# Kernel tuning notes

Measured on AMD Instinct MI355X. Metric: run time of the kernel, lower is better.

Reference implementation:

```python
import jax, jax.numpy as jnp
import numpy as np

N_NODES = 50000
N_EDGES = 600000
IN_DIM = 128
HID_DIM = 128
OUT_DIM = 128
N_GRAPHS = 64


def _glorot(key, shape):
    lim = np.sqrt(6.0 / (shape[0] + shape[1]))
    return jax.random.uniform(key, shape, jnp.float32, -lim, lim)


def setup_inputs() -> dict:
    key = jax.random.key(0)
    ks = jax.random.split(key, 8)
    h = jax.random.normal(ks[0], (N_NODES, IN_DIM), jnp.float32)
    src = jax.random.randint(ks[1], (N_EDGES,), 0, N_NODES, jnp.int64)
    dst = jax.random.randint(ks[2], (N_EDGES,), 0, N_NODES, jnp.int64)
    graph_ids = jnp.sort(jax.random.randint(ks[3], (N_NODES,), 0, N_GRAPHS, jnp.int64))
    W1 = _glorot(ks[4], (IN_DIM, HID_DIM)); b1 = jnp.zeros((HID_DIM,), jnp.float32)
    W2 = _glorot(ks[5], (HID_DIM, HID_DIM)); b2 = jnp.zeros((HID_DIM,), jnp.float32)
    W3 = _glorot(ks[6], (HID_DIM, OUT_DIM)); b3 = jnp.zeros((OUT_DIM,), jnp.float32)
    return {"h": h, "src": src, "dst": dst, "graph_ids": graph_ids,
            "W1": W1, "b1": b1, "W2": W2, "b2": b2, "W3": W3, "b3": b3,
            "n_graphs": N_GRAPHS}


def _graph_conv(h, src, dst, norm_src, norm_dst, W, b):
    # DGL GraphConv, norm='both': D_dst^{-1/2} A^T D_src^{-1/2} h W + b
    m = h * norm_src[:, None]                                   # [N, d]
    agg = jax.ops.segment_sum(m[src], dst, num_segments=h.shape[0])  # [N, d]
    return (agg * norm_dst[:, None]) @ W + b


def reference(h, src, dst, graph_ids, W1, b1, W2, b2, W3, b3, n_graphs):
    n = h.shape[0]
    ones = jnp.ones((src.shape[0],), h.dtype)
    out_deg = jnp.clip(jax.ops.segment_sum(ones, src, num_segments=n), 1.0)
    in_deg = jnp.clip(jax.ops.segment_sum(ones, dst, num_segments=n), 1.0)
    norm_src = out_deg ** -0.5
    norm_dst = in_deg ** -0.5

    x = jax.nn.relu(_graph_conv(h, src, dst, norm_src, norm_dst, W1, b1))
    x = jax.nn.relu(_graph_conv(x, src, dst, norm_src, norm_dst, W2, b2))
    x = jax.nn.relu(_graph_conv(x, src, dst, norm_src, norm_dst, W3, b3))

    # dgl.mean_nodes: per-graph mean over nodes
    gsum = jax.ops.segment_sum(x, graph_ids, num_segments=n_graphs)          # [G, d]
    gcnt = jax.ops.segment_sum(jnp.ones((n,), x.dtype), graph_ids, num_segments=n_graphs)
    return gsum / jnp.clip(gcnt, 1.0)[:, None]
```

## Files before the change

### kernel.cpp

```cpp
#include <hip/hip_runtime.h>
#include <hip/hip_fp16.h>


#define DIM 128
#define GRAPHS 64

typedef _Float16 half8 __attribute__((ext_vector_type(8)));
typedef _Float16 half4 __attribute__((ext_vector_type(4)));
typedef float floatx4 __attribute__((ext_vector_type(4)));

#define HIST_R 4
#define HIST_S 64
#define NPR 12500
#define LDSW (NPR / 2)

__global__ __launch_bounds__(256) void k_hist(const int* __restrict__ src,
                                              const int* __restrict__ dst,
                                              unsigned* __restrict__ partial, int E) {
    __shared__ unsigned hist[LDSW];
    int b = blockIdx.x;
    int a = b / (HIST_R * HIST_S);
    int r = (b / HIST_S) % HIST_R;
    int s = b % HIST_S;
    const int* arr = a ? dst : src;
    for (int i = threadIdx.x; i < LDSW; i += 256) hist[i] = 0;
    __syncthreads();
    int chunk = (E + HIST_S - 1) / HIST_S;
    int e0 = s * chunk;
    int e1 = min(e0 + chunk, E);
    unsigned base = (unsigned)(r * NPR);
    for (int i = e0 + threadIdx.x; i < e1; i += 256) {
        unsigned n = (unsigned)arr[i] - base;
        if (n < NPR) atomicAdd(&hist[n >> 1], 1u << ((n & 1) * 16));
    }
    __syncthreads();
    unsigned* outp = partial + ((size_t)(a * HIST_R + r) * HIST_S + s) * LDSW;
    for (int i = threadIdx.x; i < LDSW; i += 256) outp[i] = hist[i];
}

__global__ __launch_bounds__(256) void k_hist_merge(const unsigned* __restrict__ partial,
                                                    float* __restrict__ ns,
                                                    float* __restrict__ nd,
                                                    int* __restrict__ inc,
                                                    int* __restrict__ bsum, int N) {
    __shared__ int sred[256];
    int nb = (N + 255) / 256;
    int isDst = (blockIdx.x < nb) ? 1 : 0;
    int cb = isDst ? blockIdx.x : blockIdx.x - nb;
    int n = cb * 256 + threadIdx.x;
    int deg = 0;
    if (n < N) {
        int a = isDst ? 1 : 0;
        int r = n / NPR;
        int w = (n % NPR) >> 1;
        int field = (n & 1) * 16;
        const unsigned* p = partial + ((size_t)(a * HIST_R + r) * HIST_S) * LDSW + w;
        unsigned sum = 0;
#pragma unroll
        for (int s = 0; s < HIST_S; ++s) sum += p[(size_t)s * LDSW];
        deg = (int)((sum >> field) & 0xFFFFu);
        float nrm = rsqrtf(fmaxf((float)deg, 1.0f));
        if (isDst) { nd[n] = nrm; inc[n] = deg; }
        else       { ns[n] = nrm; }
    }
    if (isDst) {
        sred[threadIdx.x] = deg;
        __syncthreads();
        for (int off = 128; off > 0; off >>= 1) {
            if (threadIdx.x < off) sred[threadIdx.x] += sred[threadIdx.x + off];
            __syncthreads();
        }
        if (threadIdx.x == 0) bsum[cb] = sred[0];
    }
}

__global__ __launch_bounds__(256) void k_scan_write(const int* __restrict__ inc,
                                                    const int* __restrict__ bsum,
                                                    const unsigned* __restrict__ partial,
                                                    int* __restrict__ row_ptr,
                                                    int* __restrict__ cur,
                                                    float* __restrict__ gsum, int N) {
    __shared__ int sb[256];
    __shared__ int s[256];
    __shared__ int exs[256];
    int nb = (N + 255) / 256;
    int t = threadIdx.x;

    int bv = (t < nb) ? bsum[t] : 0;
    sb[t] = bv;
    __syncthreads();
    for (int off = 1; off < 256; off <<= 1) {
        int u = (t >= off) ? sb[t - off] : 0;
        __syncthreads();
        sb[t] += u;
        __syncthreads();
    }
    int excl = sb[t] - bv;
    __syncthreads();
    sb[t] = excl;
    __syncthreads();
    int blockBase = sb[blockIdx.x];

    int B = blockIdx.x * 256;
    int i = B + t;
    int v = (i < N) ? inc[i] : 0;
    s[t] = v;
    __syncthreads();
    for (int off = 1; off < 256; off <<= 1) {
        int u = (t >= off) ? s[t - off] : 0;
        __syncthreads();
        s[t] += u;
        __syncthreads();
    }
    int ex = blockBase + s[t] - v;
    exs[t] = ex;
    if (i < N) row_ptr[i] = ex;
    if (i == N - 1) row_ptr[N] = ex + v;
    if (blockIdx.x == 0) {
        for (int j = t; j < GRAPHS * DIM; j += 256) gsum[j] = 0.0f;
    }
    __syncthreads();

    if (t < 128) {
        int n0 = B + 2 * t;
        if (n0 < N) {
            int r = n0 / NPR;
            int w = (n0 % NPR) >> 1;
            const unsigned* p = partial + ((size_t)(HIST_R + r) * HIST_S) * LDSW + w;
            int run0 = exs[2 * t];
            int run1 = exs[2 * t + 1];
            int* c = cur + (size_t)r * HIST_S * NPR + 2 * w;
#pragma unroll
            for (int sl = 0; sl < HIST_S; ++sl) {
                c[(size_t)sl * NPR + 0] = run0;
                c[(size_t)sl * NPR + 1] = run1;
                unsigned hv = p[(size_t)sl * LDSW];
                run0 += (int)(hv & 0xFFFFu);
                run1 += (int)(hv >> 16);
            }
        }
    }
}

__global__ __launch_bounds__(256) void k_fill2(const int* __restrict__ src,
                                               const int* __restrict__ dst,
                                               const int* __restrict__ cur,
                                               int* __restrict__ csr, int E) {
    __shared__ int lcur[NPR];
    int r = blockIdx.x / HIST_S;
    int s = blockIdx.x % HIST_S;
    const int* cs = cur + (size_t)(r * HIST_S + s) * NPR;
    for (int i = threadIdx.x; i < NPR; i += 256) lcur[i] = cs[i];
    __syncthreads();
    int chunk = (E + HIST_S - 1) / HIST_S;
    int e0 = s * chunk;
    int e1 = min(e0 + chunk, E);
    unsigned base = (unsigned)(r * NPR);
    for (int i = e0 + threadIdx.x; i < e1; i += 256) {
        unsigned d = (unsigned)dst[i] - base;
        if (d < NPR) {
            int p = atomicAdd(&lcur[d], 1);
            csr[p] = src[i];
        }
    }
}

__global__ void k_prep(const float4* __restrict__ h, const float* __restrict__ ns,
                       uint2* __restrict__ A,
                       const float* __restrict__ W1, const float* __restrict__ W2,
                       const float* __restrict__ W3, _Float16* __restrict__ Wt1,
                       _Float16* __restrict__ Wt2, _Float16* __restrict__ Wt3, int N) {
    int i = blockIdx.x * blockDim.x + threadIdx.x;
    int nf4 = N * 32;
    if (i < nf4) {
        int n = i >> 5;
        float s = ns[n];
        float4 v = h[i];
        __half2 p0 = __floats2half2_rn(v.x * s, v.y * s);
        __half2 p1 = __floats2half2_rn(v.z * s, v.w * s);
        uint2 o;
        o.x = *(unsigned*)&p0;
        o.y = *(unsigned*)&p1;
        A[i] = o;
    } else {
        int j = i - nf4;
        if (j < 3 * 16384) {
            int which = j >> 14;
            int local = j & 16383;
            int k = local >> 7;
            int n = local & 127;
            const float* W = (which == 0) ? W1 : (which == 1) ? W2 : W3;
            _Float16* Wt = (which == 0) ? Wt1 : (which == 1) ? Wt2 : Wt3;
            Wt[(size_t)n * DIM + k] = (_Float16)W[local];
        }
    }
}

__global__ __launch_bounds__(256) void k_agg(const uint2* __restrict__ A,
                                             const int* __restrict__ row_ptr,
                                             const int* __restrict__ csr,
                                             const float* __restrict__ nd,
                                             uint2* __restrict__ Bh, int N) {
    int gtid = blockIdx.x * blockDim.x + threadIdx.x;
    int node = gtid >> 6;
    int lane = threadIdx.x & 63;
    if (node >= N) return;
    int e0 = row_ptr[node];
    int e1 = row_ptr[node + 1];
    int half = lane >> 5;
    int l8 = lane & 31;
    float ax = 0.f, ay = 0.f, az = 0.f, aw = 0.f;

    for (int base = e0; base < e1; base += 16) {
        int vl = csr[min(base + (lane & 15), e1 - 1)];
        int idx[8];
        uint2 u[8];
#pragma unroll
        for (int j = 0; j < 8; ++j) {
            idx[j] = __shfl(vl, 2 * j + half);
        }
#pragma unroll
        for (int j = 0; j < 8; ++j) {
            u[j] = A[(size_t)idx[j] * 32 + l8];
        }
#pragma unroll
        for (int j = 0; j < 8; ++j) {
            int ee = base + 2 * j + half;
            if (ee < e1) {
                __half2 p0 = *(__half2*)&u[j].x;
                __half2 p1 = *(__half2*)&u[j].y;
                float2 f0 = __half22float2(p0);
                float2 f1 = __half22float2(p1);
                ax += f0.x; ay += f0.y; az += f1.x; aw += f1.y;
            }
        }
    }

    ax += __shfl_xor(ax, 32);
    ay += __shfl_xor(ay, 32);
    az += __shfl_xor(az, 32);
    aw += __shfl_xor(aw, 32);

    if (half == 0) {
        float scale = nd[node];
        __half2 p0 = __floats2half2_rn(ax * scale, ay * scale);
        __half2 p1 = __floats2half2_rn(az * scale, aw * scale);
        uint2 o;
        o.x = *(unsigned*)&p0;
        o.y = *(unsigned*)&p1;
        Bh[(size_t)node * 32 + l8] = o;
    }
}

template <bool SCALE_NS>
__global__ __launch_bounds__(256) void k_gemm_t(
    const _Float16* __restrict__ Bin, const _Float16* __restrict__ Wt,
    const float* __restrict__ bias, const float* __restrict__ ns,
    _Float16* __restrict__ Xout, int N) {
    int tid = threadIdx.x;
    int wave = tid >> 6;
    int lane = tid & 63;
    int quad = lane >> 4;
    int l16 = lane & 15;
    int node = blockIdx.x * 64 + wave * 16 + l16;

    half8 b[4];
#pragma unroll
    for (int q = 0; q < 4; ++q) {
        if (node < N) {
            b[q] = *(const half8*)&Bin[(size_t)node * DIM + q * 32 + quad * 8];
        } else {
            b[q] = half8{0, 0, 0, 0, 0, 0, 0, 0};
        }
    }

    floatx4 acc[8];
#pragma unroll
    for (int c = 0; c < 8; ++c) acc[c] = floatx4{0.f, 0.f, 0.f, 0.f};

#pragma unroll
    for (int c = 0; c < 8; ++c) {
#pragma unroll
        for (int q = 0; q < 4; ++q) {
            half8 a = *(const half8*)&Wt[(size_t)(c * 16 + l16) * DIM + q * 32 + quad * 8];
            acc[c] = __builtin_amdgcn_mfma_f32_16x16x32_f16(a, b[q], acc[c], 0, 0, 0);
        }
    }

    if (node < N) {
        float s = SCALE_NS ? ns[node] : 1.0f;
#pragma unroll
        for (int c = 0; c < 8; ++c) {
            float4 b4 = *(const float4*)&bias[c * 16 + quad * 4];
            half4 o;
            o[0] = (_Float16)(fmaxf(acc[c][0] + b4.x, 0.0f) * s);
            o[1] = (_Float16)(fmaxf(acc[c][1] + b4.y, 0.0f) * s);
            o[2] = (_Float16)(fmaxf(acc[c][2] + b4.z, 0.0f) * s);
            o[3] = (_Float16)(fmaxf(acc[c][3] + b4.w, 0.0f) * s);
            *(half4*)&Xout[(size_t)node * DIM + c * 16 + quad * 4] = o;
        }
    }
}

#define PBINS 8
__global__ __launch_bounds__(256) void k_gemm_pool(
    const _Float16* __restrict__ Bin, const _Float16* __restrict__ Wt,
    const float* __restrict__ bias, const int* __restrict__ gid,
    float* __restrict__ gsum, int N) {
    __shared__ float lsum[PBINS * DIM];
    int tid = threadIdx.x;
    for (int i = tid; i < PBINS * DIM; i += 256) lsum[i] = 0.0f;
    int wave = tid >> 6;
    int lane = tid & 63;
    int quad = lane >> 4;
    int l16 = lane & 15;
    int r0 = blockIdx.x * 64;
    int node = r0 + wave * 16 + l16;
    int nodec = min(node, N - 1);

    half8 b[4];
#pragma unroll
    for (int q = 0; q < 4; ++q) {
        if (node < N) {
            b[q] = *(const half8*)&Bin[(size_t)node * DIM + q * 32 + quad * 8];
        } else {
            b[q] = half8{0, 0, 0, 0, 0, 0, 0, 0};
        }
    }

    floatx4 acc[8];
#pragma unroll
    for (int c = 0; c < 8; ++c) acc[c] = floatx4{0.f, 0.f, 0.f, 0.f};
    __syncthreads();

#pragma unroll
    for (int c = 0; c < 8; ++c) {
#pragma unroll
        for (int q = 0; q < 4; ++q) {
            half8 a = *(const half8*)&Wt[(size_t)(c * 16 + l16) * DIM + q * 32 + quad * 8];
            acc[c] = __builtin_amdgcn_mfma_f32_16x16x32_f16(a, b[q], acc[c], 0, 0, 0);
        }
    }

    int g = gid[nodec];
    int g0b = gid[r0];
    int gEb = gid[min(r0 + 63, N - 1)];
    bool ldsPath = (gEb - g0b) < PBINS;
    int gF = __shfl(g, 0);
    int gL = __shfl(g, 15);
    bool uni = (gF == gL);
    float valid = (node < N) ? 1.0f : 0.0f;

#pragma unroll
    for (int c = 0; c < 8; ++c) {
        float4 b4 = *(const float4*)&bias[c * 16 + quad * 4];
        float bv[4] = {b4.x, b4.y, b4.z, b4.w};
#pragma unroll
        for (int r = 0; r < 4; ++r) {
            float v = fmaxf(acc[c][r] + bv[r], 0.0f) * valid;
            int f = c * 16 + quad * 4 + r;
            if (ldsPath) {
                if (uni) {
                    v += __shfl_xor(v, 1);
                    v += __shfl_xor(v, 2);
                    v += __shfl_xor(v, 4);
                    v += __shfl_xor(v, 8);
                    if (l16 == 0) atomicAdd(&lsum[(gF - g0b) * DIM + f], v);
                } else {
                    if (node < N) atomicAdd(&lsum[(g - g0b) * DIM + f], v);
                }
            } else {
                if (node < N) atomicAdd(&gsum[(size_t)g * DIM + f], v);
            }
        }
    }
    __syncthreads();
    if (ldsPath) {
        int ng = gEb - g0b + 1;
        for (int i = tid; i < ng * DIM; i += 256) {
            float sv = lsum[i];
            if (sv != 0.0f) atomicAdd(&gsum[(size_t)g0b * DIM + i], sv);
        }
    }
}

__global__ void k_finalize(const float* __restrict__ gsum, const int* __restrict__ gid,
                           float* __restrict__ out, int N, int G) {
    int i = blockIdx.x * blockDim.x + threadIdx.x;
    if (i < G * DIM) {
        int g = i >> 7;
        int lo = 0, hi = N;
        while (lo < hi) { int m = (lo + hi) >> 1; if (gid[m] < g) lo = m + 1; else hi = m; }
        int lo2 = lo, hi2 = N;
        while (lo2 < hi2) { int m = (lo2 + hi2) >> 1; if (gid[m] < g + 1) lo2 = m + 1; else hi2 = m; }
        float c = fmaxf((float)(lo2 - lo), 1.0f);
        out[i] = gsum[i] / c;
    }
}

extern "C" void kernel_launch(void* const* d_in, const int* in_sizes, int n_in,
                              void* d_out, int out_size, void* d_ws, size_t ws_size,
                              hipStream_t stream) {
    const float* h   = (const float*)d_in[0];
    const int*   src = (const int*)d_in[1];
    const int*   dst = (const int*)d_in[2];
    const int*   gid = (const int*)d_in[3];
    const float* W1  = (const float*)d_in[4];
    const float* b1  = (const float*)d_in[5];
    const float* W2  = (const float*)d_in[6];
    const float* b2  = (const float*)d_in[7];
    const float* W3  = (const float*)d_in[8];
    const float* b3  = (const float*)d_in[9];

    const int N = in_sizes[0] / DIM;
    const int E = in_sizes[1];
    const int G = GRAPHS;
    float* out = (float*)d_out;

    char* ws = (char*)d_ws;
    size_t off = 0;
    auto alloc = [&](size_t bytes) -> void* {
        void* p = ws + off;
        off += (bytes + 255) & ~(size_t)255;
        return p;
    };
    const int nb = (N + 255) / 256;
    uint2* Ah0     = (uint2*)alloc((size_t)N * DIM * 2);
    uint2* Ah1     = (uint2*)alloc((size_t)N * DIM * 2);
    uint2* Bh      = (uint2*)alloc((size_t)N * DIM * 2);
    _Float16* Wt1  = (_Float16*)alloc((size_t)DIM * DIM * 2);
    _Float16* Wt2  = (_Float16*)alloc((size_t)DIM * DIM * 2);
    _Float16* Wt3  = (_Float16*)alloc((size_t)DIM * DIM * 2);
    float* ns      = (float*)alloc((size_t)N * 4);
    float* nd      = (float*)alloc((size_t)N * 4);
    int*   inc     = (int*)alloc((size_t)N * 4);
    unsigned* partial = (unsigned*)alloc((size_t)2 * HIST_R * HIST_S * LDSW * 4);
    int*   cur     = (int*)alloc((size_t)HIST_R * HIST_S * NPR * 4);
    int*   row_ptr = (int*)alloc((size_t)(N + 1) * 4);
    int*   csr     = (int*)alloc((size_t)E * 4);
    float* gsum    = (float*)alloc((size_t)G * DIM * 4);
    int*   bsum    = (int*)alloc((size_t)nb * 4);

    k_hist<<<2 * HIST_R * HIST_S, 256, 0, stream>>>(src, dst, partial, E);
    k_hist_merge<<<2 * nb, 256, 0, stream>>>(partial, ns, nd, inc, bsum, N);
    k_scan_write<<<nb, 256, 0, stream>>>(inc, bsum, partial, row_ptr, cur, gsum, N);
    k_fill2<<<HIST_R * HIST_S, 256, 0, stream>>>(src, dst, cur, csr, E);

    int prepThreads = N * 32 + 3 * 16384;
    k_prep<<<(prepThreads + 255) / 256, 256, 0, stream>>>((const float4*)h, ns, Ah0,
                                                          W1, W2, W3, Wt1, Wt2, Wt3, N);

    int aggBlocks  = (N * 64 + 255) / 256;
    int gemmBlocks = (N + 63) / 64;

    k_agg<<<aggBlocks, 256, 0, stream>>>(Ah0, row_ptr, csr, nd, Bh, N);
    k_gemm_t<true><<<gemmBlocks, 256, 0, stream>>>((const _Float16*)Bh, Wt1, b1, ns, (_Float16*)Ah1, N);
    k_agg<<<aggBlocks, 256, 0, stream>>>(Ah1, row_ptr, csr, nd, Bh, N);
    k_gemm_t<true><<<gemmBlocks, 256, 0, stream>>>((const _Float16*)Bh, Wt2, b2, ns, (_Float16*)Ah0, N);
    k_agg<<<aggBlocks, 256, 0, stream>>>(Ah0, row_ptr, csr, nd, Bh, N);
    k_gemm_pool<<<gemmBlocks, 256, 0, stream>>>((const _Float16*)Bh, Wt3, b3, gid, gsum, N);

    k_finalize<<<(G * DIM + 255) / 256, 256, 0, stream>>>(gsum, gid, out, N, G);
}
```

Before: 310.2 us.

## Fuse neighbor aggregation and MFMA GEMM into one per-layer kernel via LDS tile

Each layer's gather-aggregate and dense transform are merged into a single kernel. Each block aggregates 16 nodes (4 per wave) into an LDS tile, then wave 0 runs the MFMA GEMM from that tile and writes the activated output or pools it. This drops the intermediate Bh buffer round-trip through global memory and halves the layer kernel launches. The cost is less parallelism: each wave now walks 4 nodes serially, and 3 of 4 waves sit idle during the GEMM. The pooling path also loses its LDS pre-reduction, so it issues more global atomics.

```diff
diff --git a/kernel.cpp b/kernel.cpp
--- a/kernel.cpp
+++ b/kernel.cpp
@@ -196,79 +196,84 @@
     }
 }
 
-__global__ __launch_bounds__(256) void k_agg(const uint2* __restrict__ A,
-                                             const int* __restrict__ row_ptr,
-                                             const int* __restrict__ csr,
-                                             const float* __restrict__ nd,
-                                             uint2* __restrict__ Bh, int N) {
-    int gtid = blockIdx.x * blockDim.x + threadIdx.x;
-    int node = gtid >> 6;
-    int lane = threadIdx.x & 63;
-    if (node >= N) return;
-    int e0 = row_ptr[node];
-    int e1 = row_ptr[node + 1];
-    int half = lane >> 5;
-    int l8 = lane & 31;
-    float ax = 0.f, ay = 0.f, az = 0.f, aw = 0.f;
-
-    for (int base = e0; base < e1; base += 16) {
-        int vl = csr[min(base + (lane & 15), e1 - 1)];
-        int idx[8];
-        uint2 u[8];
-#pragma unroll
-        for (int j = 0; j < 8; ++j) {
-            idx[j] = __shfl(vl, 2 * j + half);
-        }
-#pragma unroll
-        for (int j = 0; j < 8; ++j) {
-            u[j] = A[(size_t)idx[j] * 32 + l8];
-        }
-#pragma unroll
-        for (int j = 0; j < 8; ++j) {
-            int ee = base + 2 * j + half;
-            if (ee < e1) {
-                __half2 p0 = *(__half2*)&u[j].x;
-                __half2 p1 = *(__half2*)&u[j].y;
-                float2 f0 = __half22float2(p0);
-                float2 f1 = __half22float2(p1);
-                ax += f0.x; ay += f0.y; az += f1.x; aw += f1.y;
-            }
-        }
-    }
-
-    ax += __shfl_xor(ax, 32);
-    ay += __shfl_xor(ay, 32);
-    az += __shfl_xor(az, 32);
-    aw += __shfl_xor(aw, 32);
-
-    if (half == 0) {
-        float scale = nd[node];
-        __half2 p0 = __floats2half2_rn(ax * scale, ay * scale);
-        __half2 p1 = __floats2half2_rn(az * scale, aw * scale);
-        uint2 o;
-        o.x = *(unsigned*)&p0;
-        o.y = *(unsigned*)&p1;
-        Bh[(size_t)node * 32 + l8] = o;
-    }
-}
-
-template <bool SCALE_NS>
-__global__ __launch_bounds__(256) void k_gemm_t(
-    const _Float16* __restrict__ Bin, const _Float16* __restrict__ Wt,
-    const float* __restrict__ bias, const float* __restrict__ ns,
-    _Float16* __restrict__ Xout, int N) {
+#define TSTRIDE 136
+
+template <bool SCALE_NS, bool POOL>
+__global__ __launch_bounds__(256) void k_layer(
+    const uint2* __restrict__ A, const int* __restrict__ row_ptr,
+    const int* __restrict__ csr, const float* __restrict__ nd,
+    const _Float16* __restrict__ Wt, const float* __restrict__ bias,
+    const float* __restrict__ ns, const int* __restrict__ gid,
+    _Float16* __restrict__ Xout, float* __restrict__ gsum, int N) {
+    __shared__ _Float16 tile[16 * TSTRIDE];
     int tid = threadIdx.x;
     int wave = tid >> 6;
     int lane = tid & 63;
+    int r0 = blockIdx.x * 16;
+
+    int half = lane >> 5;
+    int l8 = lane & 31;
+#pragma unroll 1
+    for (int i = 0; i < 4; ++i) {
+        int nl = wave * 4 + i;
+        int node = r0 + nl;
+        if (node >= N) break;
+        int e0 = row_ptr[node];
+        int e1 = row_ptr[node + 1];
+        float ax = 0.f, ay = 0.f, az = 0.f, aw = 0.f;
+
+        for (int base = e0; base < e1; base += 16) {
+            int vl = csr[min(base + (lane & 15), e1 - 1)];
+            int idx[8];
+            uint2 u[8];
+#pragma unroll
+            for (int j = 0; j < 8; ++j) {
+                idx[j] = __shfl(vl, 2 * j + half);
+            }
+#pragma unroll
+            for (int j = 0; j < 8; ++j) {
+                u[j] = A[(size_t)idx[j] * 32 + l8];
+            }
+#pragma unroll
+            for (int j = 0; j < 8; ++j) {
+                int ee = base + 2 * j + half;
+                if (ee < e1) {
+                    __half2 p0 = *(__half2*)&u[j].x;
+                    __half2 p1 = *(__half2*)&u[j].y;
+                    float2 f0 = __half22float2(p0);
+                    float2 f1 = __half22float2(p1);
+                    ax += f0.x; ay += f0.y; az += f1.x; aw += f1.y;
+                }
+            }
+        }
+
+        ax += __shfl_xor(ax, 32);
+        ay += __shfl_xor(ay, 32);
+        az += __shfl_xor(az, 32);
+        aw += __shfl_xor(aw, 32);
+
+        if (half == 0) {
+            float scale = nd[node];
+            __half2 p0 = __floats2half2_rn(ax * scale, ay * scale);
+            __half2 p1 = __floats2half2_rn(az * scale, aw * scale);
+            uint2 o;
+            o.x = *(unsigned*)&p0;
+            o.y = *(unsigned*)&p1;
+            *(uint2*)&tile[nl * TSTRIDE + l8 * 4] = o;
+        }
+    }
+    __syncthreads();
+
+    if (wave != 0) return;
     int quad = lane >> 4;
     int l16 = lane & 15;
-    int node = blockIdx.x * 64 + wave * 16 + l16;
+    int node = r0 + l16;
 
     half8 b[4];
 #pragma unroll
     for (int q = 0; q < 4; ++q) {
         if (node < N) {
-            b[q] = *(const half8*)&Bin[(size_t)node * DIM + q * 32 + quad * 8];
+            b[q] = *(const half8*)&tile[l16 * TSTRIDE + q * 32 + quad * 8];
         } else {
             b[q] = half8{0, 0, 0, 0, 0, 0, 0, 0};
         }
@@ -287,99 +292,46 @@
         }
     }
 
-    if (node < N) {
-        float s = SCALE_NS ? ns[node] : 1.0f;
+    if (!POOL) {
+        if (node < N) {
+            float s = SCALE_NS ? ns[node] : 1.0f;
+#pragma unroll
+            for (int c = 0; c < 8; ++c) {
+                float4 b4 = *(const float4*)&bias[c * 16 + quad * 4];
+                half4 o;
+                o[0] = (_Float16)(fmaxf(acc[c][0] + b4.x, 0.0f) * s);
+                o[1] = (_Float16)(fmaxf(acc[c][1] + b4.y, 0.0f) * s);
+                o[2] = (_Float16)(fmaxf(acc[c][2] + b4.z, 0.0f) * s);
+                o[3] = (_Float16)(fmaxf(acc[c][3] + b4.w, 0.0f) * s);
+                *(half4*)&Xout[(size_t)node * DIM + c * 16 + quad * 4] = o;
+            }
+        }
+    } else {
+        int nodec = min(node, N - 1);
+        int g = gid[nodec];
+        int gF = __shfl(g, 0);
+        int gL = __shfl(g, 15);
+        bool uni = (gF == gL);
+        float valid = (node < N) ? 1.0f : 0.0f;
+
 #pragma unroll
         for (int c = 0; c < 8; ++c) {
             float4 b4 = *(const float4*)&bias[c * 16 + quad * 4];
-            half4 o;
-            o[0] = (_Float16)(fmaxf(acc[c][0] + b4.x, 0.0f) * s);
-            o[1] = (_Float16)(fmaxf(acc[c][1] + b4.y, 0.0f) * s);
-            o[2] = (_Float16)(fmaxf(acc[c][2] + b4.z, 0.0f) * s);
-            o[3] = (_Float16)(fmaxf(acc[c][3] + b4.w, 0.0f) * s);
-            *(half4*)&Xout[(size_t)node * DIM + c * 16 + quad * 4] = o;
-        }
-    }
-}
-
-#define PBINS 8
-__global__ __launch_bounds__(256) void k_gemm_pool(
-    const _Float16* __restrict__ Bin, const _Float16* __restrict__ Wt,
-    const float* __restrict__ bias, const int* __restrict__ gid,
-    float* __restrict__ gsum, int N) {
-    __shared__ float lsum[PBINS * DIM];
-    int tid = threadIdx.x;
-    for (int i = tid; i < PBINS * DIM; i += 256) lsum[i] = 0.0f;
-    int wave = tid >> 6;
-    int lane = tid & 63;
-    int quad = lane >> 4;
-    int l16 = lane & 15;
-    int r0 = blockIdx.x * 64;
-    int node = r0 + wave * 16 + l16;
-    int nodec = min(node, N - 1);
-
-    half8 b[4];
-#pragma unroll
-    for (int q = 0; q < 4; ++q) {
-        if (node < N) {
-            b[q] = *(const half8*)&Bin[(size_t)node * DIM + q * 32 + quad * 8];
-        } else {
-            b[q] = half8{0, 0, 0, 0, 0, 0, 0, 0};
-        }
-    }
-
-    floatx4 acc[8];
-#pragma unroll
-    for (int c = 0; c < 8; ++c) acc[c] = floatx4{0.f, 0.f, 0.f, 0.f};
-    __syncthreads();
-
-#pragma unroll
-    for (int c = 0; c < 8; ++c) {
-#pragma unroll
-        for (int q = 0; q < 4; ++q) {
-            half8 a = *(const half8*)&Wt[(size_t)(c * 16 + l16) * DIM + q * 32 + quad * 8];
-            acc[c] = __builtin_amdgcn_mfma_f32_16x16x32_f16(a, b[q], acc[c], 0, 0, 0);
-        }
-    }
-
-    int g = gid[nodec];
-    int g0b = gid[r0];
-    int gEb = gid[min(r0 + 63, N - 1)];
-    bool ldsPath = (gEb - g0b) < PBINS;
-    int gF = __shfl(g, 0);
-    int gL = __shfl(g, 15);
-    bool uni = (gF == gL);
-    float valid = (node < N) ? 1.0f : 0.0f;
-
-#pragma unroll
-    for (int c = 0; c < 8; ++c) {
-        float4 b4 = *(const float4*)&bias[c * 16 + quad * 4];
-        float bv[4] = {b4.x, b4.y, b4.z, b4.w};
-#pragma unroll
-        for (int r = 0; r < 4; ++r) {
-            float v = fmaxf(acc[c][r] + bv[r], 0.0f) * valid;
-            int f = c * 16 + quad * 4 + r;
-            if (ldsPath) {
+            float bv[4] = {b4.x, b4.y, b4.z, b4.w};
+#pragma unroll
+            for (int r = 0; r < 4; ++r) {
+                float v = fmaxf(acc[c][r] + bv[r], 0.0f) * valid;
+                int f = c * 16 + quad * 4 + r;
                 if (uni) {
                     v += __shfl_xor(v, 1);
                     v += __shfl_xor(v, 2);
                     v += __shfl_xor(v, 4);
                     v += __shfl_xor(v, 8);
-                    if (l16 == 0) atomicAdd(&lsum[(gF - g0b) * DIM + f], v);
+                    if (l16 == 0) atomicAdd(&gsum[(size_t)gF * DIM + f], v);
                 } else {
-                    if (node < N) atomicAdd(&lsum[(g - g0b) * DIM + f], v);
+                    if (node < N) atomicAdd(&gsum[(size_t)g * DIM + f], v);
                 }
-            } else {
-                if (node < N) atomicAdd(&gsum[(size_t)g * DIM + f], v);
-            }
-        }
-    }
-    __syncthreads();
-    if (ldsPath) {
-        int ng = gEb - g0b + 1;
-        for (int i = tid; i < ng * DIM; i += 256) {
-            float sv = lsum[i];
-            if (sv != 0.0f) atomicAdd(&gsum[(size_t)g0b * DIM + i], sv);
+            }
         }
     }
 }
@@ -427,7 +379,6 @@
     const int nb = (N + 255) / 256;
     uint2* Ah0     = (uint2*)alloc((size_t)N * DIM * 2);
     uint2* Ah1     = (uint2*)alloc((size_t)N * DIM * 2);
-    uint2* Bh      = (uint2*)alloc((size_t)N * DIM * 2);
     _Float16* Wt1  = (_Float16*)alloc((size_t)DIM * DIM * 2);
     _Float16* Wt2  = (_Float16*)alloc((size_t)DIM * DIM * 2);
     _Float16* Wt3  = (_Float16*)alloc((size_t)DIM * DIM * 2);
@@ -450,15 +401,14 @@
     k_prep<<<(prepThreads + 255) / 256, 256, 0, stream>>>((const float4*)h, ns, Ah0,
                                                           W1, W2, W3, Wt1, Wt2, Wt3, N);
 
-    int aggBlocks  = (N * 64 + 255) / 256;
-    int gemmBlocks = (N + 63) / 64;
-
-    k_agg<<<aggBlocks, 256, 0, stream>>>(Ah0, row_ptr, csr, nd, Bh, N);
-    k_gemm_t<true><<<gemmBlocks, 256, 0, stream>>>((const _Float16*)Bh, Wt1, b1, ns, (_Float16*)Ah1, N);
-    k_agg<<<aggBlocks, 256, 0, stream>>>(Ah1, row_ptr, csr, nd, Bh, N);
-    k_gemm_t<true><<<gemmBlocks, 256, 0, stream>>>((const _Float16*)Bh, Wt2, b2, ns, (_Float16*)Ah0, N);
-    k_agg<<<aggBlocks, 256, 0, stream>>>(Ah0, row_ptr, csr, nd, Bh, N);
-    k_gemm_pool<<<gemmBlocks, 256, 0, stream>>>((const _Float16*)Bh, Wt3, b3, gid, gsum, N);
+    int layerBlocks = (N + 15) / 16;
+
+    k_layer<true, false><<<layerBlocks, 256, 0, stream>>>(
+        Ah0, row_ptr, csr, nd, Wt1, b1, ns, gid, (_Float16*)Ah1, gsum, N);
+    k_layer<true, false><<<layerBlocks, 256, 0, stream>>>(
+        Ah1, row_ptr, csr, nd, Wt2, b2, ns, gid, (_Float16*)Ah0, gsum, N);
+    k_layer<false, true><<<layerBlocks, 256, 0, stream>>>(
+        Ah0, row_ptr, csr, nd, Wt3, b3, ns, gid, (_Float16*)nullptr, gsum, N);
 
     k_finalize<<<(G * DIM + 255) / 256, 256, 0, stream>>>(gsum, gid, out, N, G);
 }
```

Result: slower. 332.9 us (+7.3%).
